# Performance work log

Hardware: AMD Instinct MI355X
Metric: run time of the kernel (lower is better)

Reference implementation:

```python
import jax, jax.numpy as jnp
import numpy as np


def setup_inputs() -> dict:
    key = jax.random.key(0)
    ks = jax.random.split(key, 7)
    H, O, B, T = 256, 128, 2048, 100
    s = 1.0 / np.sqrt(H)
    return {
        "C": jax.random.normal(ks[0], (B, H), dtype=jnp.float32),
        "W_ih": jax.random.uniform(ks[1], (4 * H, H), jnp.float32, -s, s),
        "W_hh": jax.random.uniform(ks[2], (4 * H, H), jnp.float32, -s, s),
        "b_ih": jax.random.uniform(ks[3], (4 * H,), jnp.float32, -s, s),
        "b_hh": jax.random.uniform(ks[4], (4 * H,), jnp.float32, -s, s),
        "W_out": jax.random.uniform(ks[5], (O, H), jnp.float32, -s, s),
        "b_out": jax.random.uniform(ks[6], (O,), jnp.float32, -s, s),
        "max_seq_len": T,
    }


def reference(C, W_ih, W_hh, b_ih, b_hh, W_out, b_out, max_seq_len):
    B, H = C.shape
    # Input contribution is the same at every step (the module re-feeds C).
    x_gates = C @ W_ih.T + b_ih + b_hh  # [B, 4H]

    def step(carry, _):
        h, c = carry
        gates = x_gates + h @ W_hh.T  # [B, 4H]
        i, f, g, o = jnp.split(gates, 4, axis=-1)  # torch gate order: i,f,g,o
        c_new = jax.nn.sigmoid(f) * c + jax.nn.sigmoid(i) * jnp.tanh(g)
        h_new = jax.nn.sigmoid(o) * jnp.tanh(c_new)
        y = h_new @ W_out.T + b_out  # [B, O]
        return (h_new, c_new), y

    init = (jnp.zeros((B, H), C.dtype), jnp.zeros((B, H), C.dtype))
    _, ys = jax.lax.scan(step, init, None, length=max_seq_len)
    return ys  # [T, B, O]
```

## Files before the change

### kernel.cpp

```cpp
#include <hip/hip_runtime.h>
#include <hip/hip_bf16.h>

typedef __attribute__((ext_vector_type(8))) short  bf16x8;
typedef __attribute__((ext_vector_type(4))) short  s16x4;
typedef __attribute__((ext_vector_type(4))) float  f32x4;
typedef __attribute__((ext_vector_type(4))) unsigned int u32x4;

#define LOG2E 1.44269504088896340736f
template<int N> struct ic { static constexpr int v = N; };

__device__ __forceinline__ unsigned short f2bf(float x) {
    union { float f; unsigned int u; } v; v.f = x;
    unsigned int u = v.u;
    u += 0x7fffu + ((u >> 16) & 1u);
    return (unsigned short)(u >> 16);
}
__device__ __forceinline__ float fast_sigmoid(float x) {
    float e = __builtin_amdgcn_exp2f(-LOG2E * x);
    return __builtin_amdgcn_rcpf(1.0f + e);
}
__device__ __forceinline__ float fast_tanh(float x) {
    float e = __builtin_amdgcn_exp2f(2.0f * LOG2E * x);
    return 1.0f - 2.0f * __builtin_amdgcn_rcpf(1.0f + e);
}

__global__ void pack_w_big(const float* __restrict__ W, unsigned short* __restrict__ dst) {
    int idx  = blockIdx.x * 256 + threadIdx.x;
    int lane = idx & 63;
    int fid  = idx >> 6;
    int j    = fid & 7;
    int kk   = (fid >> 3) & 7;
    int w    = fid >> 6;
    int g    = j >> 1, tn = j & 1;
    int R    = g * 256 + w * 32 + tn * 16 + (lane & 15);
    int kb   = kk * 32 + 4 * (lane >> 4);
    const float* src = W + (size_t)R * 256 + kb;
    union { unsigned short s[8]; u32x4 v; } u;
#pragma unroll
    for (int e = 0; e < 8; ++e) {
        int k = (e & 3) + 16 * (e >> 2);
        u.s[e] = f2bf(src[k]);
    }
    *(u32x4*)(dst + (size_t)idx * 8) = u.v;
}

__global__ void pack_w_out(const float* __restrict__ W, unsigned short* __restrict__ dst) {
    int idx  = blockIdx.x * 256 + threadIdx.x;
    int lane = idx & 63;
    int fid  = idx >> 6;
    int kk   = fid & 7;
    int wv   = fid >> 3;
    int R    = wv * 16 + (lane & 15);
    int kb   = kk * 32 + 4 * (lane >> 4);
    const float* src = W + (size_t)R * 256 + kb;
    union { unsigned short s[8]; u32x4 v; } u;
#pragma unroll
    for (int e = 0; e < 8; ++e) {
        int k = (e & 3) + 16 * (e >> 2);
        u.s[e] = f2bf(src[k]);
    }
    *(u32x4*)(dst + (size_t)idx * 8) = u.v;
}

__global__ __launch_bounds__(512) __attribute__((amdgpu_waves_per_eu(2, 2)))
void lstm_gates(const float* __restrict__ C,
                const unsigned short* __restrict__ Wih_p,
                const unsigned short* __restrict__ Whh_p,
                const float* __restrict__ b_ih,
                const float* __restrict__ b_hh,
                unsigned short* __restrict__ H,
                int T, int Btot)
{
    __shared__ short hbuf[2][4096];
    __shared__ short park[8][8][512];
    __shared__ short ring[8][8][512];

    const int tid  = threadIdx.x;
    const int l    = tid & 63;
    const int wid  = tid >> 6;
    const int l15  = l & 15;
    const int g4   = l >> 4;
    const int row0 = blockIdx.x * 16;

    const unsigned short* wib = Wih_p + (size_t)wid * 32768;
    const unsigned short* whb = Whh_p + (size_t)wid * 32768;

    {
        int r  = tid >> 5;
        int cb = tid & 31;
        const float* src = C + (size_t)(row0 + r) * 256 + cb * 8;
        float4 f0 = *(const float4*)(src);
        float4 f1 = *(const float4*)(src + 4);
        int m  = 9 * (r & 7);
        int s0 = cb * 2;
        short* hb = hbuf[0] + r * 256;
        union { unsigned short s[4]; unsigned long long v; } p0, p1;
        p0.s[0] = f2bf(f0.x); p0.s[1] = f2bf(f0.y); p0.s[2] = f2bf(f0.z); p0.s[3] = f2bf(f0.w);
        p1.s[0] = f2bf(f1.x); p1.s[1] = f2bf(f1.y); p1.s[2] = f2bf(f1.z); p1.s[3] = f2bf(f1.w);
        *(unsigned long long*)(hb + ((s0 ^ m) * 4))       = p0.v;
        *(unsigned long long*)(hb + (((s0 + 1) ^ m) * 4)) = p1.v;
    }

    auto issueP = [&](int j) {
        const unsigned short* src = whb + (((size_t)4 * 8 + j) * 64 + l) * 8;
        __builtin_amdgcn_global_load_lds(
            (const __attribute__((address_space(1))) void*)src,
            (__attribute__((address_space(3))) void*)&park[wid][j][0], 16, 0, 0);
    };
    auto issueS = [&](int kk, int j) {
        const unsigned short* src = whb + (((size_t)kk * 8 + j) * 64 + l) * 8;
        __builtin_amdgcn_global_load_lds(
            (const __attribute__((address_space(1))) void*)src,
            (__attribute__((address_space(3))) void*)&ring[wid][j][0], 16, 0, 0);
    };
#pragma unroll
    for (int j = 0; j < 8; ++j) issueP(j);
#pragma unroll
    for (int j = 0; j < 8; ++j) issueS(5, j);

    const int msw = 9 * (l15 & 7);
    auto loadA = [&](const short* buf, int kk) -> bf16x8 {
        int slo = kk * 8 + g4;
        const short* base = buf + l15 * 256;
        s16x4 lo = *(const s16x4*)(base + ((slo ^ msw) * 4));
        s16x4 hi = *(const s16x4*)(base + (((slo + 4) ^ msw) * 4));
        bf16x8 a;
        a[0] = lo[0]; a[1] = lo[1]; a[2] = lo[2]; a[3] = lo[3];
        a[4] = hi[0]; a[5] = hi[1]; a[6] = hi[2]; a[7] = hi[3];
        return a;
    };
    auto loadB = [&](const unsigned short* wb, int kk, int j) -> bf16x8 {
        return *(const bf16x8*)(wb + (((size_t)kk * 8 + j) * 64 + l) * 8);
    };

    __syncthreads();

    f32x4 acc[8];
#pragma unroll
    for (int j = 0; j < 8; ++j) acc[j] = (f32x4){0.f, 0.f, 0.f, 0.f};
#pragma unroll
    for (int kk = 0; kk < 8; ++kk) {
        bf16x8 a = loadA(hbuf[0], kk);
#pragma unroll
        for (int j = 0; j < 8; ++j)
            acc[j] = __builtin_amdgcn_mfma_f32_16x16x32_bf16(a, loadB(wib, kk, j), acc[j], 0, 0, 0);
    }
#pragma unroll
    for (int j = 0; j < 8; ++j) {
        int g = j >> 1, tn = j & 1;
        int col = g * 256 + wid * 32 + tn * 16 + l15;
        float bias = b_ih[col] + b_hh[col];
        acc[j] = acc[j] + bias;
    }
    unsigned xgp[16];
#pragma unroll
    for (int j = 0; j < 8; ++j) {
        xgp[2 * j]     = (unsigned)f2bf(acc[j][0]) | ((unsigned)f2bf(acc[j][1]) << 16);
        xgp[2 * j + 1] = (unsigned)f2bf(acc[j][2]) | ((unsigned)f2bf(acc[j][3]) << 16);
    }
    auto xgu = [&](int j) -> f32x4 {
        union { unsigned u; float f; } c0, c1, c2, c3;
        unsigned u0 = xgp[2 * j], u1 = xgp[2 * j + 1];
        c0.u = u0 << 16; c1.u = u0 & 0xffff0000u;
        c2.u = u1 << 16; c3.u = u1 & 0xffff0000u;
        return (f32x4){c0.f, c1.f, c2.f, c3.f};
    };

    bf16x8 whr[4][8];
#pragma unroll
    for (int kk = 0; kk < 4; ++kk)
#pragma unroll
        for (int j = 0; j < 8; ++j) whr[kk][j] = loadB(whb, kk, j);

    float cst[8];
#pragma unroll
    for (int i = 0; i < 8; ++i) cst[i] = 0.f;

    auto update_write = [&](short* nxtb) {
#pragma unroll
        for (int tn = 0; tn < 2; ++tn) {
#pragma unroll
            for (int rr = 0; rr < 4; ++rr) {
                float iv = fast_sigmoid(acc[0 + tn][rr]);
                float fv = fast_sigmoid(acc[2 + tn][rr]);
                float gv = fast_tanh(acc[4 + tn][rr]);
                float ov = fast_sigmoid(acc[6 + tn][rr]);
                float cn = fv * cst[tn * 4 + rr] + iv * gv;
                cst[tn * 4 + rr] = cn;
                float hn = ov * fast_tanh(cn);
                unsigned short hb = f2bf(hn);
                int row = 4 * g4 + rr;
                int col = wid * 32 + tn * 16 + l15;
                int ps  = (col >> 2) ^ (9 * (row & 7));
                nxtb[row * 256 + ps * 4 + (col & 3)] = (short)hb;
            }
        }
    };

    auto store_h = [&](const short* srcb, unsigned short* dst) {
        int r  = tid >> 5;
        int cb = tid & 31;
        int m  = 9 * (r & 7);
        const short* hb = srcb + r * 256;
        union { s16x4 h[2]; u32x4 v; } u;
        u.h[0] = *(const s16x4*)(hb + (((cb * 2)     ^ m) * 4));
        u.h[1] = *(const s16x4*)(hb + (((cb * 2 + 1) ^ m) * 4));
        __builtin_nontemporal_store(u.v, (u32x4*)(dst + (size_t)r * 256 + cb * 8));
    };

    update_write(hbuf[1]);
    __syncthreads();

    auto phaseR0 = [&](const short* curb) {
        bf16x8 a = loadA(curb, 0);
#pragma unroll
        for (int j = 0; j < 8; ++j)
            acc[j] = __builtin_amdgcn_mfma_f32_16x16x32_bf16(a, whr[0][j], xgu(j), 0, 0, 0);
    };
    auto phaseR = [&](auto KK, const short* curb) {
        constexpr int kk = decltype(KK)::v;
        bf16x8 a = loadA(curb, kk);
#pragma unroll
        for (int j = 0; j < 8; ++j)
            acc[j] = __builtin_amdgcn_mfma_f32_16x16x32_bf16(a, whr[kk][j], acc[j], 0, 0, 0);
    };
    auto phaseP = [&](const short* curb) {
        bf16x8 a = loadA(curb, 4);
#pragma unroll
        for (int j = 0; j < 8; ++j) {
            bf16x8 b = *(const bf16x8*)&park[wid][j][l * 8];
            acc[j] = __builtin_amdgcn_mfma_f32_16x16x32_bf16(a, b, acc[j], 0, 0, 0);
        }
    };
    auto phaseS = [&](auto KK, auto NX, auto WT, const short* curb) {
        constexpr int kk = decltype(KK)::v;
        constexpr int nx = decltype(NX)::v;
        constexpr int wt = decltype(WT)::v;
        bf16x8 a = loadA(curb, kk);
        if constexpr (wt == 5) asm volatile("s_waitcnt vmcnt(5)" ::: "memory");
        else                   asm volatile("s_waitcnt vmcnt(4)" ::: "memory");
#pragma unroll
        for (int j = 0; j < 4; ++j) {
            bf16x8 b = *(const bf16x8*)&ring[wid][j][l * 8];
            acc[j] = __builtin_amdgcn_mfma_f32_16x16x32_bf16(a, b, acc[j], 0, 0, 0);
        }
#pragma unroll
        for (int j = 0; j < 4; ++j) issueS(nx, j);
        if constexpr (wt == 5) asm volatile("s_waitcnt vmcnt(5)" ::: "memory");
        else                   asm volatile("s_waitcnt vmcnt(4)" ::: "memory");
#pragma unroll
        for (int j = 4; j < 8; ++j) {
            bf16x8 b = *(const bf16x8*)&ring[wid][j][l * 8];
            acc[j] = __builtin_amdgcn_mfma_f32_16x16x32_bf16(a, b, acc[j], 0, 0, 0);
        }
#pragma unroll
        for (int j = 4; j < 8; ++j) issueS(nx, j);
    };

    for (int t = 2; t <= T; ++t) {
        const short* curb = hbuf[(t - 1) & 1];
        short*       nxtb = hbuf[t & 1];

        phaseR0(curb);
        phaseR(ic<1>{}, curb);
        phaseR(ic<2>{}, curb);
        phaseR(ic<3>{}, curb);
        phaseP(curb);
        phaseS(ic<5>{}, ic<6>{}, ic<5>{}, curb);
        phaseS(ic<6>{}, ic<7>{}, ic<4>{}, curb);
        phaseS(ic<7>{}, ic<5>{}, ic<4>{}, curb);

        store_h(curb, H + ((size_t)(t - 2) * Btot + row0) * 256);

        update_write(nxtb);

        asm volatile("s_waitcnt lgkmcnt(0)" ::: "memory");
        __builtin_amdgcn_sched_barrier(0);
        __builtin_amdgcn_s_barrier();
    }

    store_h(hbuf[T & 1], H + ((size_t)(T - 1) * Btot + row0) * 256);
}

__global__ __launch_bounds__(512) void out_gemm(
    const unsigned short* __restrict__ Wout_p,
    const float* __restrict__ b_out,
    float* __restrict__ Y)
{
    const int tid = threadIdx.x;
    const int l   = tid & 63;
    const int w   = tid >> 6;
    const int l15 = l & 15;
    const int g4  = l >> 4;
    const size_t rw0 = (size_t)blockIdx.x * 256 + w * 32;
    const unsigned short* Hp = (const unsigned short*)Y;

    bf16x8 a[2][8];
#pragma unroll
    for (int rt = 0; rt < 2; ++rt)
#pragma unroll
        for (int kk = 0; kk < 8; ++kk) {
            const unsigned short* src = Hp + (rw0 + rt * 16 + l15) * 256 + kk * 32 + 4 * g4;
            s16x4 lo = *(const s16x4*)(src);
            s16x4 hi = *(const s16x4*)(src + 16);
            bf16x8 v;
            v[0] = lo[0]; v[1] = lo[1]; v[2] = lo[2]; v[3] = lo[3];
            v[4] = hi[0]; v[5] = hi[1]; v[6] = hi[2]; v[7] = hi[3];
            a[rt][kk] = v;
        }

    f32x4 acc[2][8];
#pragma unroll
    for (int rt = 0; rt < 2; ++rt)
#pragma unroll
        for (int wv = 0; wv < 8; ++wv) acc[rt][wv] = (f32x4){0.f, 0.f, 0.f, 0.f};

#pragma unroll
    for (int kk = 0; kk < 8; ++kk)
#pragma unroll
        for (int wv = 0; wv < 8; ++wv) {
            bf16x8 wf = *(const bf16x8*)(Wout_p + ((size_t)(wv * 8 + kk) * 64 + l) * 8);
            acc[0][wv] = __builtin_amdgcn_mfma_f32_16x16x32_bf16(a[0][kk], wf, acc[0][wv], 0, 0, 0);
            acc[1][wv] = __builtin_amdgcn_mfma_f32_16x16x32_bf16(a[1][kk], wf, acc[1][wv], 0, 0, 0);
        }

#pragma unroll
    for (int wv = 0; wv < 8; ++wv) {
        float by = b_out[wv * 16 + l15];
#pragma unroll
        for (int rt = 0; rt < 2; ++rt)
#pragma unroll
            for (int i = 0; i < 4; ++i)
                Y[(rw0 + rt * 16 + 4 * g4 + i) * 128 + wv * 16 + l15] = acc[rt][wv][i] + by;
    }
}

extern "C" void kernel_launch(void* const* d_in, const int* in_sizes, int n_in,
                              void* d_out, int out_size, void* d_ws, size_t ws_size,
                              hipStream_t stream) {
    const float* C     = (const float*)d_in[0];
    const float* W_ih  = (const float*)d_in[1];
    const float* W_hh  = (const float*)d_in[2];
    const float* b_ih  = (const float*)d_in[3];
    const float* b_hh  = (const float*)d_in[4];
    const float* W_out = (const float*)d_in[5];
    const float* b_out = (const float*)d_in[6];

    const int H    = 256;
    const int Btot = in_sizes[0] / H;
    const int O    = in_sizes[5] / H;
    const int T    = out_size / (Btot * O);

    unsigned short* Whh_p  = (unsigned short*)d_ws;
    unsigned short* Wih_p  = Whh_p + (1 << 18);
    unsigned short* Wout_p = Wih_p + (1 << 18);

    hipLaunchKernelGGL(pack_w_big, dim3(128), dim3(256), 0, stream, W_hh, Whh_p);
    hipLaunchKernelGGL(pack_w_big, dim3(128), dim3(256), 0, stream, W_ih, Wih_p);
    hipLaunchKernelGGL(pack_w_out, dim3(16),  dim3(256), 0, stream, W_out, Wout_p);
    hipLaunchKernelGGL(lstm_gates, dim3(Btot / 16), dim3(512), 0, stream,
                       C, Wih_p, Whh_p, b_ih, b_hh,
                       (unsigned short*)d_out, T, Btot);
    hipLaunchKernelGGL(out_gemm, dim3((T * Btot) / 256), dim3(512), 0, stream,
                       Wout_p, b_out, (float*)d_out);
}
```

Before: 681.3 us.

## Replace park/ring weight staging with two rotating LDS buffers streaming four K-slices

The kernel previously kept K-slice 4 of W_hh resident in a 'park' LDS buffer and streamed slices 5-7 through a single 'ring' buffer. It now streams slices 4-7 through two alternating LDS buffers and interleaves them with the register-resident slices 0-3. The global h store moves earlier in the step. The goal is to give each global-to-LDS weight load a full compute phase of latency hiding and to spread the waits more evenly. In exchange, more weight bytes are reloaded from global/L2 every timestep, since slice 4 is no longer resident.

```diff
diff --git a/kernel.cpp b/kernel.cpp
--- a/kernel.cpp
+++ b/kernel.cpp
@@ -72,8 +72,8 @@
                 int T, int Btot)
 {
     __shared__ short hbuf[2][4096];
-    __shared__ short park[8][8][512];
-    __shared__ short ring[8][8][512];
+    __shared__ short bufA[8][8][512];
+    __shared__ short bufB[8][8][512];
 
     const int tid  = threadIdx.x;
     const int l    = tid & 63;
@@ -101,22 +101,16 @@
         *(unsigned long long*)(hb + (((s0 + 1) ^ m) * 4)) = p1.v;
     }
 
-    auto issueP = [&](int j) {
-        const unsigned short* src = whb + (((size_t)4 * 8 + j) * 64 + l) * 8;
-        __builtin_amdgcn_global_load_lds(
-            (const __attribute__((address_space(1))) void*)src,
-            (__attribute__((address_space(3))) void*)&park[wid][j][0], 16, 0, 0);
-    };
-    auto issueS = [&](int kk, int j) {
+    auto issueTo = [&](short (*dst)[512], int kk, int j) {
         const unsigned short* src = whb + (((size_t)kk * 8 + j) * 64 + l) * 8;
         __builtin_amdgcn_global_load_lds(
             (const __attribute__((address_space(1))) void*)src,
-            (__attribute__((address_space(3))) void*)&ring[wid][j][0], 16, 0, 0);
-    };
-#pragma unroll
-    for (int j = 0; j < 8; ++j) issueP(j);
-#pragma unroll
-    for (int j = 0; j < 8; ++j) issueS(5, j);
+            (__attribute__((address_space(3))) void*)&dst[j][0], 16, 0, 0);
+    };
+#pragma unroll
+    for (int j = 0; j < 8; ++j) issueTo(bufA[wid], 4, j);
+#pragma unroll
+    for (int j = 0; j < 8; ++j) issueTo(bufB[wid], 5, j);
 
     const int msw = 9 * (l15 & 7);
     auto loadA = [&](const short* buf, int kk) -> bf16x8 {
@@ -211,12 +205,6 @@
     update_write(hbuf[1]);
     __syncthreads();
 
-    auto phaseR0 = [&](const short* curb) {
-        bf16x8 a = loadA(curb, 0);
-#pragma unroll
-        for (int j = 0; j < 8; ++j)
-            acc[j] = __builtin_amdgcn_mfma_f32_16x16x32_bf16(a, whr[0][j], xgu(j), 0, 0, 0);
-    };
     auto phaseR = [&](auto KK, const short* curb) {
         constexpr int kk = decltype(KK)::v;
         bf16x8 a = loadA(curb, kk);
@@ -224,53 +212,37 @@
         for (int j = 0; j < 8; ++j)
             acc[j] = __builtin_amdgcn_mfma_f32_16x16x32_bf16(a, whr[kk][j], acc[j], 0, 0, 0);
     };
-    auto phaseP = [&](const short* curb) {
-        bf16x8 a = loadA(curb, 4);
+    auto phaseS = [&](auto KK, auto SEED, short (*buf)[512], auto NXKK, const short* curb) {
+        constexpr int kk   = decltype(KK)::v;
+        constexpr int seed = decltype(SEED)::v;
+        constexpr int nx   = decltype(NXKK)::v;
+        bf16x8 a = loadA(curb, kk);
+        asm volatile("s_waitcnt vmcnt(8)" ::: "memory");
 #pragma unroll
         for (int j = 0; j < 8; ++j) {
-            bf16x8 b = *(const bf16x8*)&park[wid][j][l * 8];
-            acc[j] = __builtin_amdgcn_mfma_f32_16x16x32_bf16(a, b, acc[j], 0, 0, 0);
+            bf16x8 b = *(const bf16x8*)&buf[j][l * 8];
+            if constexpr (seed)
+                acc[j] = __builtin_amdgcn_mfma_f32_16x16x32_bf16(a, b, xgu(j), 0, 0, 0);
+            else
+                acc[j] = __builtin_amdgcn_mfma_f32_16x16x32_bf16(a, b, acc[j], 0, 0, 0);
         }
-    };
-    auto phaseS = [&](auto KK, auto NX, auto WT, const short* curb) {
-        constexpr int kk = decltype(KK)::v;
-        constexpr int nx = decltype(NX)::v;
-        constexpr int wt = decltype(WT)::v;
-        bf16x8 a = loadA(curb, kk);
-        if constexpr (wt == 5) asm volatile("s_waitcnt vmcnt(5)" ::: "memory");
-        else                   asm volatile("s_waitcnt vmcnt(4)" ::: "memory");
-#pragma unroll
-        for (int j = 0; j < 4; ++j) {
-            bf16x8 b = *(const bf16x8*)&ring[wid][j][l * 8];
-            acc[j] = __builtin_amdgcn_mfma_f32_16x16x32_bf16(a, b, acc[j], 0, 0, 0);
-        }
-#pragma unroll
-        for (int j = 0; j < 4; ++j) issueS(nx, j);
-        if constexpr (wt == 5) asm volatile("s_waitcnt vmcnt(5)" ::: "memory");
-        else                   asm volatile("s_waitcnt vmcnt(4)" ::: "memory");
-#pragma unroll
-        for (int j = 4; j < 8; ++j) {
-            bf16x8 b = *(const bf16x8*)&ring[wid][j][l * 8];
-            acc[j] = __builtin_amdgcn_mfma_f32_16x16x32_bf16(a, b, acc[j], 0, 0, 0);
-        }
-#pragma unroll
-        for (int j = 4; j < 8; ++j) issueS(nx, j);
+#pragma unroll
+        for (int j = 0; j < 8; ++j) issueTo(buf, nx, j);
     };
 
     for (int t = 2; t <= T; ++t) {
         const short* curb = hbuf[(t - 1) & 1];
         short*       nxtb = hbuf[t & 1];
 
-        phaseR0(curb);
+        phaseS(ic<4>{}, ic<1>{}, bufA[wid], ic<6>{}, curb);
+        phaseS(ic<5>{}, ic<0>{}, bufB[wid], ic<7>{}, curb);
+        store_h(curb, H + ((size_t)(t - 2) * Btot + row0) * 256);
+        phaseR(ic<0>{}, curb);
         phaseR(ic<1>{}, curb);
+        phaseS(ic<6>{}, ic<0>{}, bufA[wid], ic<4>{}, curb);
+        phaseS(ic<7>{}, ic<0>{}, bufB[wid], ic<5>{}, curb);
         phaseR(ic<2>{}, curb);
         phaseR(ic<3>{}, curb);
-        phaseP(curb);
-        phaseS(ic<5>{}, ic<6>{}, ic<5>{}, curb);
-        phaseS(ic<6>{}, ic<7>{}, ic<4>{}, curb);
-        phaseS(ic<7>{}, ic<5>{}, ic<4>{}, curb);
-
-        store_h(curb, H + ((size_t)(t - 2) * Btot + row0) * 256);
 
         update_write(nxtb);
 
```

Measured after the change: 804.1 us. 18.0% more time.

## Replicate streamed W_hh slices across workspace copies to spread load traffic

Applied to the files above, without the earlier changes.

Adds a kernel that copies the streamed portion of the packed W_hh (k-blocks 5..7) into up to 128 replicas in workspace. Each LSTM block then streams its per-step ring weights from the replica selected by its block index instead of all blocks reading the same addresses. This spreads the repeated per-timestep weight reads over many address ranges to reduce contention on the same cache lines and channels. The cost is an extra replication kernel, a larger workspace footprint, and a higher overall cache footprint.

```diff
diff --git a/kernel.cpp b/kernel.cpp
--- a/kernel.cpp
+++ b/kernel.cpp
@@ -62,14 +62,30 @@
     *(u32x4*)(dst + (size_t)idx * 8) = u.v;
 }
 
+__global__ void replicate_stream(const unsigned short* __restrict__ Whh_p,
+                                 unsigned short* __restrict__ rep) {
+    int gidx = blockIdx.x * 256 + threadIdx.x;
+    int q    = gidx % 12288;
+    int c    = gidx / 12288;
+    int lane = q & 63;
+    int f    = q >> 6;
+    int j    = f & 7;
+    int kkp  = (f >> 3) % 3;
+    int w    = f / 24;
+    const u32x4* src = (const u32x4*)(Whh_p + (((size_t)w * 64 + (5 + kkp) * 8 + j) * 64 + lane) * 8);
+    u32x4 v = *src;
+    __builtin_nontemporal_store(v, (u32x4*)(rep + (size_t)c * 98304 + (size_t)q * 8));
+}
+
 __global__ __launch_bounds__(512) __attribute__((amdgpu_waves_per_eu(2, 2)))
 void lstm_gates(const float* __restrict__ C,
                 const unsigned short* __restrict__ Wih_p,
                 const unsigned short* __restrict__ Whh_p,
+                const unsigned short* __restrict__ rep,
                 const float* __restrict__ b_ih,
                 const float* __restrict__ b_hh,
                 unsigned short* __restrict__ H,
-                int T, int Btot)
+                int T, int Btot, int ncopies)
 {
     __shared__ short hbuf[2][4096];
     __shared__ short park[8][8][512];
@@ -84,6 +100,8 @@
 
     const unsigned short* wib = Wih_p + (size_t)wid * 32768;
     const unsigned short* whb = Whh_p + (size_t)wid * 32768;
+    const unsigned short* wstr = rep + (size_t)(blockIdx.x % ncopies) * 98304
+                                     + (size_t)wid * 12288;
 
     {
         int r  = tid >> 5;
@@ -108,7 +126,7 @@
             (__attribute__((address_space(3))) void*)&park[wid][j][0], 16, 0, 0);
     };
     auto issueS = [&](int kk, int j) {
-        const unsigned short* src = whb + (((size_t)kk * 8 + j) * 64 + l) * 8;
+        const unsigned short* src = wstr + ((size_t)((kk - 5) * 8 + j) * 64 + l) * 8;
         __builtin_amdgcn_global_load_lds(
             (const __attribute__((address_space(1))) void*)src,
             (__attribute__((address_space(3))) void*)&ring[wid][j][0], 16, 0, 0);
@@ -351,16 +369,26 @@
     const int O    = in_sizes[5] / H;
     const int T    = out_size / (Btot * O);
 
-    unsigned short* Whh_p  = (unsigned short*)d_ws;
-    unsigned short* Wih_p  = Whh_p + (1 << 18);
-    unsigned short* Wout_p = Wih_p + (1 << 18);
+    char* ws = (char*)d_ws;
+    unsigned short* Whh_p  = (unsigned short*)(ws);
+    unsigned short* Wih_p  = (unsigned short*)(ws + (512 << 10));
+    unsigned short* Wout_p = (unsigned short*)(ws + (1024 << 10));
+    unsigned short* rep    = (unsigned short*)(ws + (1088 << 10));
+
+    const size_t copy_bytes = 196608;
+    size_t avail = (ws_size > (1088u << 10)) ? ws_size - (1088u << 10) : 0;
+    int ncopies = (int)(avail / copy_bytes);
+    if (ncopies > 128) ncopies = 128;
+    if (ncopies < 1)   ncopies = 1;
 
     hipLaunchKernelGGL(pack_w_big, dim3(128), dim3(256), 0, stream, W_hh, Whh_p);
     hipLaunchKernelGGL(pack_w_big, dim3(128), dim3(256), 0, stream, W_ih, Wih_p);
     hipLaunchKernelGGL(pack_w_out, dim3(16),  dim3(256), 0, stream, W_out, Wout_p);
+    hipLaunchKernelGGL(replicate_stream, dim3(ncopies * 48), dim3(256), 0, stream,
+                       Whh_p, rep);
     hipLaunchKernelGGL(lstm_gates, dim3(Btot / 16), dim3(512), 0, stream,
-                       C, Wih_p, Whh_p, b_ih, b_hh,
-                       (unsigned short*)d_out, T, Btot);
+                       C, Wih_p, Whh_p, rep, b_ih, b_hh,
+                       (unsigned short*)d_out, T, Btot, ncopies);
     hipLaunchKernelGGL(out_gemm, dim3((T * Btot) / 256), dim3(512), 0, stream,
                        Wout_p, b_out, (float*)d_out);
 }
```

Result: slower. 1.017 ms (+49.2%).
